# Kernel tuning notes

Hardware: AMD Instinct MI355X
Metric: run time of the kernel (lower is better)

Reference implementation:

```python
import math
import jax, jax.numpy as jnp
import numpy as np

B, T, C, H, V = 2, 512, 768, 12, 50304
HD = C // H
EPS_LN = 1e-5
SINK_ITERS = 6           # MAX_ITER_SINK
N_STEPS = 20             # ceil((1-0)/h_max), h_max=0.05
H_STEP = 1.0 / N_STEPS   # Euler step size h


def layer_norm(x, w, b):
    mu = jnp.mean(x, axis=-1, keepdims=True)
    var = jnp.mean(jnp.square(x - mu), axis=-1, keepdims=True)
    return (x - mu) * jax.lax.rsqrt(var + EPS_LN) * w + b


def sinkhorn_pi(Cmat):
    # log-domain Sinkhorn (eps=1) on cost matrix Cmat [N, T, T]; returns transport plan pi
    n = Cmat.shape[-1]
    log_marg = -jnp.log(jnp.asarray(n, Cmat.dtype))  # log(1/n), uniform marginals
    u = jnp.zeros(Cmat.shape[:-1], Cmat.dtype)
    v = jnp.zeros(Cmat.shape[:-1], Cmat.dtype)
    def M(u, v):
        return -Cmat + u[..., :, None] + v[..., None, :]
    for _ in range(SINK_ITERS):
        u = (log_marg - jax.nn.logsumexp(M(u, v), axis=-1)) + u
        v = (log_marg - jax.nn.logsumexp(M(u, v), axis=-2)) + v
    return jnp.exp(M(u, v))


def block_f(z, t, attn_ln_w, attn_ln_b, c_attn_w, c_attn_b, c_proj_w, c_proj_b,
            mlp_ln_w, mlp_ln_b, c_fc_w, c_fc_b, mlp_proj_w, mlp_proj_b):
    Bz, Tz, Cz = z.shape
    tcol = jnp.full((Bz, Tz, 1), t, z.dtype)
    # attention sub-block: LN over C+1 dims (x concat time)
    x = layer_norm(jnp.concatenate([z, tcol], axis=-1), attn_ln_w, attn_ln_b)
    qkv = x @ c_attn_w + c_attn_b                      # [B,T,3C]
    q, k, v = jnp.split(qkv, 3, axis=-1)
    q = q.reshape(Bz, Tz, H, HD).transpose(0, 2, 1, 3)  # [B,H,T,hd]
    k = k.reshape(Bz, Tz, H, HD).transpose(0, 2, 1, 3)
    v = v.reshape(Bz, Tz, H, HD).transpose(0, 2, 1, 3)
    att = jnp.einsum('bhqd,bhkd->bhqk', q, k) * (1.0 / math.sqrt(HD))
    mask = jnp.tril(jnp.ones((Tz, Tz), dtype=bool))
    att = jax.nn.softmax(jnp.where(mask, att, -jnp.inf), axis=-1)
    pi = sinkhorn_pi(att.reshape(Bz * H, Tz, Tz)) * Tz  # sink(att)[0] * n
    y = jnp.einsum('bhqk,bhkd->bhqd', pi.reshape(Bz, H, Tz, Tz), v)
    y = y.transpose(0, 2, 1, 3).reshape(Bz, Tz, Cz)
    y = y @ c_proj_w + c_proj_b
    # MLP sub-block on LN(concat(attn_out, t))
    ht = layer_norm(jnp.concatenate([y, tcol], axis=-1), mlp_ln_w, mlp_ln_b)
    h1 = jax.nn.gelu(ht @ c_fc_w + c_fc_b, approximate=False)
    return h1 @ mlp_proj_w + mlp_proj_b


def setup_inputs() -> dict:
    key = jax.random.key(0)
    ks = jax.random.split(key, 8)
    s = 0.02
    return {
        'idx': jax.random.randint(ks[0], (B, T), 0, V),
        'wte': s * jax.random.normal(ks[1], (V, C), jnp.float32),
        'wpe': s * jax.random.normal(ks[2], (T, C), jnp.float32),
        'attn_ln_w': jnp.ones((C + 1,), jnp.float32),
        'attn_ln_b': jnp.zeros((C + 1,), jnp.float32),
        'c_attn_w': s * jax.random.normal(ks[3], (C + 1, 3 * C), jnp.float32),
        'c_attn_b': jnp.zeros((3 * C,), jnp.float32),
        'c_proj_w': s * jax.random.normal(ks[4], (C, C), jnp.float32),
        'c_proj_b': jnp.zeros((C,), jnp.float32),
        'mlp_ln_w': jnp.ones((C + 1,), jnp.float32),
        'mlp_ln_b': jnp.zeros((C + 1,), jnp.float32),
        'c_fc_w': s * jax.random.normal(ks[5], (C + 1, 4 * C), jnp.float32),
        'c_fc_b': jnp.zeros((4 * C,), jnp.float32),
        'mlp_proj_w': s * jax.random.normal(ks[6], (4 * C, C), jnp.float32),
        'mlp_proj_b': jnp.zeros((C,), jnp.float32),
        'lnf_w': jnp.ones((C,), jnp.float32),
        'lnf_b': jnp.zeros((C,), jnp.float32),
    }


def reference(idx, wte, wpe, attn_ln_w, attn_ln_b, c_attn_w, c_attn_b, c_proj_w,
              c_proj_b, mlp_ln_w, mlp_ln_b, c_fc_w, c_fc_b, mlp_proj_w, mlp_proj_b,
              lnf_w, lnf_b):
    x = wte[idx] + wpe[jnp.arange(idx.shape[1])]  # [B,T,C]

    def step(carry, _):
        z, t = carry
        dz = block_f(z, t, attn_ln_w, attn_ln_b, c_attn_w, c_attn_b, c_proj_w,
                     c_proj_b, mlp_ln_w, mlp_ln_b, c_fc_w, c_fc_b, mlp_proj_w,
                     mlp_proj_b)
        return (z + H_STEP * dz, t + H_STEP), None

    (x, _), _ = jax.lax.scan(step, (x, jnp.float32(0.0)), None, length=N_STEPS)
    x = layer_norm(x, lnf_w, lnf_b)
    logits = x[:, -1:, :] @ wte.T  # inference path: last position only, tied head
    return logits
```

## Files before the change

kernel.cpp:

```cpp
#include <hip/hip_runtime.h>
#include <hip/hip_bf16.h>
#include <math.h>

typedef unsigned short ushortT;
typedef unsigned int uintT;

#define Bc   2
#define Tc   512
#define Cc   768
#define Hc   12
#define HDc  64
#define Vc   50304
#define BTc  (Bc*Tc)
#define NHc  (Bc*Hc)
#define C3   (3*Cc)
#define C4   (4*Cc)
#define EPS_LN 1e-5f
#define H_STEP 0.05f
#define INVN (1.0f/512.0f)
#define SB   4
#define ELP  (Tc + 8)
#define VLP  136

typedef float f32x4 __attribute__((ext_vector_type(4)));
typedef __bf16 bf16x8 __attribute__((ext_vector_type(8)));
typedef ushortT us8 __attribute__((ext_vector_type(8)));
typedef uintT u32x4 __attribute__((ext_vector_type(4)));

__device__ __forceinline__ ushortT f2bf(float f) {
    union { float f; unsigned u; } x; x.f = f;
    unsigned r = (x.u + 0x7fffu + ((x.u >> 16) & 1u)) >> 16;
    return (ushortT)r;
}
__device__ __forceinline__ float bf2f(ushortT b) {
    union { unsigned u; float f; } x; x.u = ((unsigned)b) << 16;
    return x.f;
}
__device__ __forceinline__ float bflo(uintT w) {
    union { unsigned u; float f; } x; x.u = w << 16;
    return x.f;
}
__device__ __forceinline__ float bfhi(uintT w) {
    union { unsigned u; float f; } x; x.u = w & 0xffff0000u;
    return x.f;
}

__device__ __forceinline__ void gll16(const ushortT* g, ushortT* l) {
    __builtin_amdgcn_global_load_lds(
        (const __attribute__((address_space(1))) unsigned int*)g,
        (__attribute__((address_space(3))) unsigned int*)l,
        16, 0, 0);
}

__device__ __forceinline__ float waveReduceSumX(float v) {
    for (int o = 32; o; o >>= 1) v += __shfl_xor(v, o);
    return v;
}
__device__ __forceinline__ float blockReduceSum(float v) {
    __shared__ float sm[4];
    for (int o = 32; o; o >>= 1) v += __shfl_down(v, o);
    __syncthreads();
    if ((threadIdx.x & 63) == 0) sm[threadIdx.x >> 6] = v;
    __syncthreads();
    return sm[0] + sm[1] + sm[2] + sm[3];
}

__global__ __launch_bounds__(256)
void wtrans_kernel(const float* __restrict__ W, ushortT* __restrict__ out,
                   int K, int N)
{
    __shared__ float t[32][33];
    int k0 = blockIdx.x * 32, n0 = blockIdx.y * 32;
    int tx = threadIdx.x & 31, ty = threadIdx.x >> 5;
    for (int r = ty; r < 32; r += 8)
        t[r][tx] = W[(size_t)(k0 + r) * N + n0 + tx];
    __syncthreads();
    for (int r = ty; r < 32; r += 8)
        out[(size_t)(n0 + r) * K + k0 + tx] = f2bf(t[tx][r]);
}

__global__ __launch_bounds__(256)
void embed_ln(const int* __restrict__ idx, const float* __restrict__ wte,
              const float* __restrict__ wpe, float* __restrict__ z,
              const float* __restrict__ lnw, const float* __restrict__ lnb,
              ushortT* __restrict__ xlnb, float* __restrict__ xt)
{
    int row = blockIdx.x, tid = threadIdx.x;
    int tok = idx[row];
    float v[3];
#pragma unroll
    for (int q = 0; q < 3; ++q) {
        int c = tid + 256 * q;
        float val = wte[(size_t)tok * Cc + c] + wpe[(size_t)(row & (Tc - 1)) * Cc + c];
        z[(size_t)row * Cc + c] = val;
        v[q] = val;
    }
    float s = blockReduceSum(v[0] + v[1] + v[2]);
    float mu = s / 769.f;
    float d0 = v[0] - mu, d1 = v[1] - mu, d2 = v[2] - mu;
    float ss = blockReduceSum(d0 * d0 + d1 * d1 + d2 * d2);
    float dt = 0.f - mu;
    float var = (ss + dt * dt) / 769.f;
    float rs = rsqrtf(var + EPS_LN);
#pragma unroll
    for (int q = 0; q < 3; ++q) {
        int c = tid + 256 * q;
        xlnb[(size_t)row * Cc + c] = f2bf((v[q] - mu) * rs * lnw[c] + lnb[c]);
    }
    if (tid == 0) xt[row] = dt * rs * lnw[Cc] + lnb[Cc];
}

__global__ __launch_bounds__(256)
void ln_kernel(const void* __restrict__ X, const float* __restrict__ w,
               const float* __restrict__ bb, void* __restrict__ Y,
               float* __restrict__ yt, int hasT, float tval,
               int rowMul, int rowAdd, int obf16, int ibf16)
{
    int orow = blockIdx.x;
    int r = orow * rowMul + rowAdd;
    int tid = threadIdx.x;
    float xv[3];
    if (ibf16) {
        const ushortT* x = (const ushortT*)X + (size_t)r * Cc;
#pragma unroll
        for (int q = 0; q < 3; ++q) xv[q] = bf2f(x[tid + 256 * q]);
    } else {
        const float* x = (const float*)X + (size_t)r * Cc;
#pragma unroll
        for (int q = 0; q < 3; ++q) xv[q] = x[tid + 256 * q];
    }
    float s = blockReduceSum(xv[0] + xv[1] + xv[2]);
    float cnt = hasT ? 769.f : 768.f;
    float mu = (s + (hasT ? tval : 0.f)) / cnt;
    float d0 = xv[0] - mu, d1 = xv[1] - mu, d2 = xv[2] - mu;
    float ss = blockReduceSum(d0 * d0 + d1 * d1 + d2 * d2);
    float dt = tval - mu;
    float var = (ss + (hasT ? dt * dt : 0.f)) / cnt;
    float rs = rsqrtf(var + EPS_LN);
#pragma unroll
    for (int q = 0; q < 3; ++q) {
        int c = tid + 256 * q;
        float v = (xv[q] - mu) * rs * w[c] + bb[c];
        if (obf16) ((ushortT*)Y)[(size_t)orow * Cc + c] = f2bf(v);
        else       ((float*)Y)[(size_t)orow * Cc + c] = v;
    }
    if (hasT && tid == 0) yt[orow] = dt * rs * w[Cc] + bb[Cc];
}

template <int EPI>
__global__ __launch_bounds__(256)
void gemm_bt(const ushortT* __restrict__ A, int lda,
             const ushortT* __restrict__ Bt, int ldb,
             void* __restrict__ Cm, int ldc, int K,
             const float* __restrict__ bias,
             const float* __restrict__ extraA,
             const float* __restrict__ extraB)
{
    __shared__ __align__(16) ushortT Als[128 * 64];
    __shared__ __align__(16) ushortT Bls[128 * 64];
    if (EPI == 4) {
        int koff = blockIdx.z * K;
        A += koff; Bt += koff;
    }
    int tid = threadIdx.x;
    int lane = tid & 63, wid = tid >> 6;
    int wm = wid >> 1, wn = wid & 1;
    int m0 = blockIdx.y * 128, n0 = blockIdx.x * 128;
    f32x4 acc[4][4];
    const f32x4 fz = {0.f, 0.f, 0.f, 0.f};
#pragma unroll
    for (int i = 0; i < 4; ++i)
#pragma unroll
        for (int j = 0; j < 4; ++j) acc[i][j] = fz;

    for (int k0 = 0; k0 < K; k0 += 64) {
#pragma unroll
        for (int is = 0; is < 4; ++is) {
            int ch = is * 256 + tid;
            int m = ch >> 3;
            int kc8 = (ch & 7) ^ (m & 7);
            gll16(A + (size_t)(m0 + m) * lda + k0 + kc8 * 8, Als + ch * 8);
            gll16(Bt + (size_t)(n0 + m) * ldb + k0 + kc8 * 8, Bls + ch * 8);
        }
        __syncthreads();
#pragma unroll
        for (int kk = 0; kk < 2; ++kk) {
            int cidx = kk * 4 + (lane >> 4);
            bf16x8 af[4], bfv[4];
#pragma unroll
            for (int i = 0; i < 4; ++i) {
                int row = wm * 64 + i * 16 + (lane & 15);
                af[i] = *(const bf16x8*)(Als + ((size_t)row * 8 + (cidx ^ (row & 7))) * 8);
                int col = wn * 64 + i * 16 + (lane & 15);
                bfv[i] = *(const bf16x8*)(Bls + ((size_t)col * 8 + (cidx ^ (col & 7))) * 8);
            }
#pragma unroll
            for (int i = 0; i < 4; ++i)
#pragma unroll
                for (int j = 0; j < 4; ++j)
                    acc[i][j] = __builtin_amdgcn_mfma_f32_16x16x32_bf16(af[i], bfv[j], acc[i][j], 0, 0, 0);
        }
        __syncthreads();
    }
#pragma unroll
    for (int i = 0; i < 4; ++i) {
#pragma unroll
        for (int j = 0; j < 4; ++j) {
#pragma unroll
            for (int r = 0; r < 4; ++r) {
                int row = m0 + wm * 64 + i * 16 + (lane >> 4) * 4 + r;
                int col = n0 + wn * 64 + j * 16 + (lane & 15);
                float v = acc[i][j][r];
                if (extraA) v += extraA[row] * extraB[col];
                if (bias) v += bias[col];
                size_t oi = (size_t)row * ldc + col;
                if (EPI == 0) {
                    ((ushortT*)Cm)[oi] = f2bf(v);
                } else if (EPI == 1) {
                    v = 0.5f * v * (1.f + erff(v * 0.70710678118654752440f));
                    ((ushortT*)Cm)[oi] = f2bf(v);
                } else if (EPI == 4) {
                    ((float*)Cm)[(size_t)blockIdx.z * ((size_t)BTc * Cc) + oi] = v;
                }
            }
        }
    }
}

__global__ __launch_bounds__(512)
void sinkfused(const ushortT* __restrict__ qkvb, ushortT* __restrict__ y,
               float* __restrict__ partials, unsigned* __restrict__ ctr,
               unsigned barBase)
{
    int gb = blockIdx.x;
    int n = gb % NHc, r = gb / NHc;
    int row0 = r * 128;
    int b = n / Hc, h = n - b * Hc;
    int tid = threadIdx.x;
    int l = tid & 63, w = tid >> 6;
    __shared__ __align__(16) ushortT Els[128][ELP];
    __shared__ __align__(16) ushortT Kshare[64 * VLP];
    __shared__ float a_s[128];
    __shared__ float b_s[Tc];
    const f32x4 fz = {0.f, 0.f, 0.f, 0.f};

    int qrow = b * Tc + row0 + w * 16 + (l & 15);
    const ushortT* qp = qkvb + (size_t)qrow * C3 + h * HDc + (l >> 4) * 8;
    bf16x8 aq0 = *(const bf16x8*)(qp);
    bf16x8 aq1 = *(const bf16x8*)(qp + 32);

    int kcmax = r + 1;
    f32x4 acc[32];
#pragma unroll
    for (int j = 0; j < 32; ++j) acc[j] = fz;

    ushortT* EK = &Els[0][0];
    {
        int nch = kcmax * 1024;
        for (int ch = tid; ch < nch; ch += 512) {
            int row = ch >> 3, c16 = (ch & 7) ^ (row & 7);
            gll16(qkvb + (size_t)(b * Tc + row) * C3 + Cc + h * HDc + c16 * 8,
                  EK + ch * 8);
        }
    }
    __syncthreads();
#pragma unroll
    for (int kc = 0; kc < 4; ++kc) {
        if (kc < kcmax) {
#pragma unroll
            for (int jj = 0; jj < 8; ++jj) {
                int krow = kc * 128 + jj * 16 + (l & 15);
                int c16a = (l >> 4);
                int c16b = 4 + (l >> 4);
                bf16x8 bk0 = *(const bf16x8*)(EK + ((size_t)krow * 8 + (c16a ^ (krow & 7))) * 8);
                bf16x8 bk1 = *(const bf16x8*)(EK + ((size_t)krow * 8 + (c16b ^ (krow & 7))) * 8);
                acc[kc * 8 + jj] = __builtin_amdgcn_mfma_f32_16x16x32_bf16(aq0, bk0, acc[kc * 8 + jj], 0, 0, 0);
                acc[kc * 8 + jj] = __builtin_amdgcn_mfma_f32_16x16x32_bf16(aq1, bk1, acc[kc * 8 + jj], 0, 0, 0);
            }
        }
    }
    __syncthreads();

    int nvalid = kcmax * 8;
    int colbase = (l & 15);
    int rowa[4];
#pragma unroll
    for (int e = 0; e < 4; ++e) rowa[e] = row0 + w * 16 + (l >> 4) * 4 + e;

    float mx[4] = {-INFINITY, -INFINITY, -INFINITY, -INFINITY};
#pragma unroll
    for (int j = 0; j < 32; ++j) {
        if (j < nvalid) {
            int col = j * 16 + colbase;
#pragma unroll
            for (int e = 0; e < 4; ++e)
                if (col <= rowa[e]) mx[e] = fmaxf(mx[e], acc[j][e] * 0.125f);
        }
    }
#pragma unroll
    for (int e = 0; e < 4; ++e)
        for (int o = 1; o < 16; o <<= 1) mx[e] = fmaxf(mx[e], __shfl_xor(mx[e], o));

    float se[4] = {0.f, 0.f, 0.f, 0.f};
#pragma unroll
    for (int j = 0; j < 32; ++j) {
        if (j < nvalid) {
            int col = j * 16 + colbase;
#pragma unroll
            for (int e = 0; e < 4; ++e) {
                float exv = (col <= rowa[e]) ? __expf(acc[j][e] * 0.125f - mx[e]) : 0.f;
                acc[j][e] = exv;
                se[e] += exv;
            }
        }
    }
#pragma unroll
    for (int e = 0; e < 4; ++e)
        for (int o = 1; o < 16; o <<= 1) se[e] += __shfl_xor(se[e], o);
    float inv[4];
#pragma unroll
    for (int e = 0; e < 4; ++e) inv[e] = 1.f / se[e];

    float rsum[4] = {0.f, 0.f, 0.f, 0.f};
#pragma unroll
    for (int j = 0; j < 32; ++j) {
        if (j < nvalid) {
            int col = j * 16 + colbase;
#pragma unroll
            for (int e = 0; e < 4; ++e) {
                float Ee = __expf(-(acc[j][e] * inv[e]));
                rsum[e] += Ee;
                Els[w * 16 + (l >> 4) * 4 + e][col] = f2bf(Ee);
            }
        }
    }
#pragma unroll
    for (int e = 0; e < 4; ++e) {
        for (int o = 1; o < 16; o <<= 1) rsum[e] += __shfl_xor(rsum[e], o);
        if ((l & 15) == 0)
            a_s[w * 16 + (l >> 4) * 4 + e] = INVN / (rsum[e] + (float)(Tc - nvalid * 16));
    }
    {
        int tailc = 64 - kcmax * 16;
        if (tailc > 0) {
            us8 ones8;
#pragma unroll
            for (int e = 0; e < 8; ++e) ones8[e] = 0x3F80;
            for (int idx2 = l; idx2 < 16 * tailc; idx2 += 64) {
                int rr = idx2 / tailc, cc = idx2 - rr * tailc;
                *(us8*)&Els[w * 16 + rr][(kcmax * 16 + cc) * 8] = ones8;
            }
        }
    }
    __syncthreads();

    float* mypart = partials + (size_t)(n * SB + r) * Tc;
    const float* hpart = partials + (size_t)n * SB * Tc;
    unsigned* myctr = ctr + n * 16;
    float* scr = (float*)Kshare;

#pragma unroll 1
    for (int p = 0; p < 11; ++p) {
        if ((p & 1) == 0) {
            int cg = tid & 63, sl = tid >> 6;
            float ac[8] = {0.f, 0.f, 0.f, 0.f, 0.f, 0.f, 0.f, 0.f};
#pragma unroll
            for (int i = 0; i < 16; ++i) {
                int row = sl * 16 + i;
                us8 ev = *(const us8*)&Els[row][cg * 8];
                float fa = a_s[row];
#pragma unroll
                for (int e = 0; e < 8; ++e)
                    ac[e] += bf2f(ev[e]) * fa;
            }
            f32x4 lo = {ac[0], ac[1], ac[2], ac[3]};
            f32x4 hi = {ac[4], ac[5], ac[6], ac[7]};
            *(f32x4*)&scr[sl * 512 + cg * 8] = lo;
            *(f32x4*)&scr[sl * 512 + cg * 8 + 4] = hi;
            __syncthreads();
            int j = tid;
            float accs = 0.f;
#pragma unroll
            for (int s2 = 0; s2 < 8; ++s2) accs += scr[s2 * 512 + j];
            __hip_atomic_store(&mypart[j], accs, __ATOMIC_RELAXED, __HIP_MEMORY_SCOPE_AGENT);
            __syncthreads();
            if (tid == 0) {
                __threadfence();
                atomicAdd(myctr, 1u);
                unsigned tgt = barBase + (unsigned)(p / 2 + 1) * SB;
                while (__hip_atomic_load(myctr, __ATOMIC_ACQUIRE, __HIP_MEMORY_SCOPE_AGENT) < tgt)
                    __builtin_amdgcn_s_sleep(2);
            }
            __syncthreads();
            float s0 = __hip_atomic_load(&hpart[j], __ATOMIC_RELAXED, __HIP_MEMORY_SCOPE_AGENT);
            float s1 = __hip_atomic_load(&hpart[Tc + j], __ATOMIC_RELAXED, __HIP_MEMORY_SCOPE_AGENT);
            float s2 = __hip_atomic_load(&hpart[2 * Tc + j], __ATOMIC_RELAXED, __HIP_MEMORY_SCOPE_AGENT);
            float s3 = __hip_atomic_load(&hpart[3 * Tc + j], __ATOMIC_RELAXED, __HIP_MEMORY_SCOPE_AGENT);
            b_s[j] = INVN / (s0 + s1 + s2 + s3);
            __syncthreads();
        } else {
            f32x4 b0 = *(const f32x4*)&b_s[l * 8];
            f32x4 b1 = *(const f32x4*)&b_s[l * 8 + 4];
            float breg[8] = {b0[0], b0[1], b0[2], b0[3], b1[0], b1[1], b1[2], b1[3]};
#pragma unroll 1
            for (int k = 0; k < 16; k += 4) {
                int r0 = w * 16 + k;
                u32x4 q0 = *(const u32x4*)(&Els[r0 + 0][l * 8]);
                u32x4 q1 = *(const u32x4*)(&Els[r0 + 1][l * 8]);
                u32x4 q2 = *(const u32x4*)(&Els[r0 + 2][l * 8]);
                u32x4 q3 = *(const u32x4*)(&Els[r0 + 3][l * 8]);
                float s0 = 0.f, s1 = 0.f, s2 = 0.f, s3 = 0.f;
#pragma unroll
                for (int c = 0; c < 4; ++c) {
                    s0 += bflo(q0[c]) * breg[2 * c] + bfhi(q0[c]) * breg[2 * c + 1];
                    s1 += bflo(q1[c]) * breg[2 * c] + bfhi(q1[c]) * breg[2 * c + 1];
                    s2 += bflo(q2[c]) * breg[2 * c] + bfhi(q2[c]) * breg[2 * c + 1];
                    s3 += bflo(q3[c]) * breg[2 * c] + bfhi(q3[c]) * breg[2 * c + 1];
                }
                s0 = waveReduceSumX(s0);
                s1 = waveReduceSumX(s1);
                s2 = waveReduceSumX(s2);
                s3 = waveReduceSumX(s3);
                if (l == 0) {
                    a_s[r0 + 0] = INVN / s0;
                    a_s[r0 + 1] = INVN / s1;
                    a_s[r0 + 2] = INVN / s2;
                    a_s[r0 + 3] = INVN / s3;
                }
            }
            __syncthreads();
        }
    }

    {
        ushortT* Kls2 = Kshare;
        int wm = w >> 1, wn = w & 1;
        f32x4 acc2[2][2];
#pragma unroll
        for (int i = 0; i < 2; ++i)
#pragma unroll
            for (int j = 0; j < 2; ++j) acc2[i][j] = fz;
        const ushortT* vbase = qkvb + (size_t)(b * Tc) * C3 + 2 * Cc + h * HDc;

#pragma unroll 1
        for (int k0 = 0; k0 < Tc; k0 += 128) {
#pragma unroll
            for (int ii = 0; ii < 2; ++ii) {
                int ch = ii * 512 + tid;
                int tt = ch >> 3, dblk = ch & 7;
                us8 vv = *(const us8*)(vbase + (size_t)(k0 + tt) * C3 + dblk * 8);
                float bs = 512.f * b_s[k0 + tt];
#pragma unroll
                for (int e = 0; e < 8; ++e)
                    Kls2[(dblk * 8 + e) * VLP + tt] = f2bf(bf2f(vv[e]) * bs);
            }
            __syncthreads();
#pragma unroll
            for (int kk = 0; kk < 128; kk += 32) {
                bf16x8 af[2], bv[2];
#pragma unroll
                for (int i = 0; i < 2; ++i)
                    af[i] = *(const bf16x8*)&Els[wm * 32 + i * 16 + (l & 15)][k0 + kk + (l >> 4) * 8];
#pragma unroll
                for (int j = 0; j < 2; ++j)
                    bv[j] = *(const bf16x8*)(Kls2 + (size_t)(wn * 32 + j * 16 + (l & 15)) * VLP + kk + (l >> 4) * 8);
#pragma unroll
                for (int i = 0; i < 2; ++i)
#pragma unroll
                    for (int j = 0; j < 2; ++j)
                        acc2[i][j] = __builtin_amdgcn_mfma_f32_16x16x32_bf16(af[i], bv[j], acc2[i][j], 0, 0, 0);
            }
            __syncthreads();
        }
#pragma unroll
        for (int i = 0; i < 2; ++i)
#pragma unroll
            for (int j = 0; j < 2; ++j)
#pragma unroll
                for (int rr = 0; rr < 4; ++rr) {
                    int lrow = wm * 32 + i * 16 + (l >> 4) * 4 + rr;
                    float a_r = a_s[lrow];
                    int grow = b * Tc + row0 + lrow;
                    int gcol = h * HDc + wn * 32 + j * 16 + (l & 15);
                    y[(size_t)grow * Cc + gcol] = f2bf(acc2[i][j][rr] * a_r);
                }
    }
}

__global__ __launch_bounds__(256)
void reduce_ln(const float* __restrict__ parts, const float* __restrict__ bias,
               float* __restrict__ z, const float* __restrict__ lnw,
               const float* __restrict__ lnb, ushortT* __restrict__ xlnb,
               float* __restrict__ xt, float tval, int doEuler)
{
    int row = blockIdx.x, tid = threadIdx.x;
    const size_t CS = (size_t)BTc * Cc;
    float v[3];
#pragma unroll
    for (int q = 0; q < 3; ++q) {
        int c = tid + 256 * q;
        size_t idx = (size_t)row * Cc + c;
        float s = parts[idx] + parts[CS + idx] + parts[2 * CS + idx]
                + parts[3 * CS + idx] + bias[c];
        if (doEuler) {
            v[q] = z[idx] + H_STEP * s;
            z[idx] = v[q];
        } else {
            v[q] = s;
        }
    }
    float s = blockReduceSum(v[0] + v[1] + v[2]);
    float mu = (s + tval) / 769.f;
    float d0 = v[0] - mu, d1 = v[1] - mu, d2 = v[2] - mu;
    float ss = blockReduceSum(d0 * d0 + d1 * d1 + d2 * d2);
    float dt = tval - mu;
    float var = (ss + dt * dt) / 769.f;
    float rs = rsqrtf(var + EPS_LN);
#pragma unroll
    for (int q = 0; q < 3; ++q) {
        int c = tid + 256 * q;
        xlnb[(size_t)row * Cc + c] = f2bf((v[q] - mu) * rs * lnw[c] + lnb[c]);
    }
    if (tid == 0) xt[row] = dt * rs * lnw[Cc] + lnb[Cc];
}

__global__ __launch_bounds__(256)
void logits_kernel(const float* __restrict__ xf, const float* __restrict__ wte,
                   float* __restrict__ out)
{
    __shared__ __align__(16) float xs[2 * Cc];
    int tid = threadIdx.x;
    for (int i = tid; i < 384; i += 256)
        ((f32x4*)xs)[i] = ((const f32x4*)xf)[i];
    __syncthreads();
    int w = tid >> 6, lane = tid & 63;
    int vrow = blockIdx.x * 4 + w;
    const f32x4* wr = (const f32x4*)(wte + (size_t)vrow * Cc);
    const f32x4* x0 = (const f32x4*)xs;
    const f32x4* x1 = (const f32x4*)(xs + Cc);
    float a0 = 0.f, a1 = 0.f;
#pragma unroll
    for (int it = 0; it < 3; ++it) {
        int k4 = it * 64 + lane;
        f32x4 wv = wr[k4];
        f32x4 p = x0[k4], q = x1[k4];
        a0 += wv[0] * p[0] + wv[1] * p[1] + wv[2] * p[2] + wv[3] * p[3];
        a1 += wv[0] * q[0] + wv[1] * q[1] + wv[2] * q[2] + wv[3] * q[3];
    }
    for (int o = 32; o; o >>= 1) {
        a0 += __shfl_down(a0, o);
        a1 += __shfl_down(a1, o);
    }
    if (lane == 0) {
        out[vrow] = a0;
        out[Vc + vrow] = a1;
    }
}

extern "C" void kernel_launch(void* const* d_in, const int* in_sizes, int n_in,
                              void* d_out, int out_size, void* d_ws, size_t ws_size,
                              hipStream_t stream)
{
    const int*   idx        = (const int*)  d_in[0];
    const float* wte        = (const float*)d_in[1];
    const float* wpe        = (const float*)d_in[2];
    const float* attn_ln_w  = (const float*)d_in[3];
    const float* attn_ln_b  = (const float*)d_in[4];
    const float* c_attn_w   = (const float*)d_in[5];
    const float* c_attn_b   = (const float*)d_in[6];
    const float* c_proj_w   = (const float*)d_in[7];
    const float* c_proj_b   = (const float*)d_in[8];
    const float* mlp_ln_w   = (const float*)d_in[9];
    const float* mlp_ln_b   = (const float*)d_in[10];
    const float* c_fc_w     = (const float*)d_in[11];
    const float* c_fc_b     = (const float*)d_in[12];
    const float* mlp_proj_w = (const float*)d_in[13];
    const float* mlp_proj_b = (const float*)d_in[14];
    const float* lnf_w      = (const float*)d_in[15];
    const float* lnf_b      = (const float*)d_in[16];
    float* out = (float*)d_out;

    char* base = (char*)d_ws;
    size_t off = 0;
    auto alloc = [&](size_t bytes) -> void* {
        void* p = base + off;
        off = (off + bytes + 255) & ~(size_t)255;
        return p;
    };
    float*   z     = (float*)  alloc((size_t)BTc * Cc * 4);
    float*   parts = (float*)  alloc((size_t)4 * BTc * Cc * 4);
    ushortT* qkvb  = (ushortT*)alloc((size_t)BTc * C3 * 2);
    ushortT* xlnb  = (ushortT*)alloc((size_t)BTc * Cc * 2);
    ushortT* y     = (ushortT*)alloc((size_t)BTc * Cc * 2);
    ushortT* h1    = (ushortT*)alloc((size_t)BTc * C4 * 2);
    float*   xt    = (float*)  alloc(BTc * 4);
    float*   partv = (float*)  alloc((size_t)NHc * SB * Tc * 4);
    unsigned* ctr  = (unsigned*)alloc(NHc * 16 * 4);
    float*   xf    = (float*)  alloc(2 * Cc * 4);
    ushortT* WqkvT = (ushortT*)alloc((size_t)C3 * Cc * 2);
    ushortT* WprojT= (ushortT*)alloc((size_t)Cc * Cc * 2);
    ushortT* WfcT  = (ushortT*)alloc((size_t)C4 * Cc * 2);
    ushortT* WmlpT = (ushortT*)alloc((size_t)Cc * C4 * 2);

    hipMemsetAsync(ctr, 0, NHc * 16 * 4, stream);
    embed_ln<<<BTc, 256, 0, stream>>>(idx, wte, wpe, z, attn_ln_w, attn_ln_b, xlnb, xt);
    wtrans_kernel<<<dim3(Cc / 32, C3 / 32), 256, 0, stream>>>(c_attn_w,   WqkvT,  Cc, C3);
    wtrans_kernel<<<dim3(Cc / 32, Cc / 32), 256, 0, stream>>>(c_proj_w,   WprojT, Cc, Cc);
    wtrans_kernel<<<dim3(Cc / 32, C4 / 32), 256, 0, stream>>>(c_fc_w,     WfcT,   Cc, C4);
    wtrans_kernel<<<dim3(C4 / 32, Cc / 32), 256, 0, stream>>>(mlp_proj_w, WmlpT,  C4, Cc);

    float t = 0.f;
    for (int step = 0; step < 20; ++step) {
        gemm_bt<0><<<dim3(C3 / 128, BTc / 128), 256, 0, stream>>>(
            xlnb, Cc, WqkvT, Cc, qkvb, C3, Cc,
            c_attn_b, xt, c_attn_w + (size_t)Cc * C3);
        sinkfused<<<NHc * SB, 512, 0, stream>>>(
            qkvb, y, partv, ctr, (unsigned)(step * 6 * SB));
        gemm_bt<4><<<dim3(Cc / 128, BTc / 128, 4), 256, 0, stream>>>(
            y, Cc, WprojT, Cc, parts, Cc, Cc / 4,
            nullptr, nullptr, nullptr);
        reduce_ln<<<BTc, 256, 0, stream>>>(parts, c_proj_b, nullptr,
                                           mlp_ln_w, mlp_ln_b, xlnb, xt, t, 0);
        gemm_bt<1><<<dim3(C4 / 128, BTc / 128), 256, 0, stream>>>(
            xlnb, Cc, WfcT, Cc, h1, C4, Cc,
            c_fc_b, xt, c_fc_w + (size_t)Cc * C4);
        gemm_bt<4><<<dim3(Cc / 128, BTc / 128, 4), 256, 0, stream>>>(
            h1, C4, WmlpT, C4, parts, Cc, C4 / 4,
            nullptr, nullptr, nullptr);
        t += H_STEP;
        reduce_ln<<<BTc, 256, 0, stream>>>(parts, mlp_proj_b, z,
                                           attn_ln_w, attn_ln_b, xlnb, xt, t, 1);
    }

    ln_kernel<<<2, 256, 0, stream>>>(z, lnf_w, lnf_b, xf, nullptr, 0, 0.f, Tc, Tc - 1, 0, 0);
    logits_kernel<<<Vc / 4, 256, 0, stream>>>(xf, wte, out);
}
```

Baseline: 3.426 ms.

## Split Sinkhorn kernel into 64-row strips across 8 blocks per head

```diff
diff --git a/kernel.cpp b/kernel.cpp
--- a/kernel.cpp
+++ b/kernel.cpp
@@ -18,7 +18,7 @@
 #define EPS_LN 1e-5f
 #define H_STEP 0.05f
 #define INVN (1.0f/512.0f)
-#define SB   4
+#define SBQ  8
 #define ELP  (Tc + 8)
 #define VLP  136
 
@@ -234,29 +234,31 @@
 {
     int gb = blockIdx.x;
     int n = gb % NHc, r = gb / NHc;
-    int row0 = r * 128;
+    int row0 = r * 64;
     int b = n / Hc, h = n - b * Hc;
     int tid = threadIdx.x;
     int l = tid & 63, w = tid >> 6;
-    __shared__ __align__(16) ushortT Els[128][ELP];
+    int wm = w >> 1, wn = w & 1;
+    __shared__ __align__(16) ushortT Els[64][ELP];
     __shared__ __align__(16) ushortT Kshare[64 * VLP];
-    __shared__ float a_s[128];
+    __shared__ float a_s[64];
     __shared__ float b_s[Tc];
+    __shared__ float smx[2][64], ssum[2][64], srs[2][64];
     const f32x4 fz = {0.f, 0.f, 0.f, 0.f};
 
-    int qrow = b * Tc + row0 + w * 16 + (l & 15);
+    int qrow = b * Tc + row0 + wm * 16 + (l & 15);
     const ushortT* qp = qkvb + (size_t)qrow * C3 + h * HDc + (l >> 4) * 8;
     bf16x8 aq0 = *(const bf16x8*)(qp);
     bf16x8 aq1 = *(const bf16x8*)(qp + 32);
 
-    int kcmax = r + 1;
-    f32x4 acc[32];
-#pragma unroll
-    for (int j = 0; j < 32; ++j) acc[j] = fz;
+    int nT2 = (r + 1) * 2;
+    f32x4 acc[16];
+#pragma unroll
+    for (int j = 0; j < 16; ++j) acc[j] = fz;
 
     ushortT* EK = &Els[0][0];
     {
-        int nch = kcmax * 1024;
+        int nch = (r + 1) * 512;
         for (int ch = tid; ch < nch; ch += 512) {
             int row = ch >> 3, c16 = (ch & 7) ^ (row & 7);
             gll16(qkvb + (size_t)(b * Tc + row) * C3 + Cc + h * HDc + c16 * 8,
@@ -265,51 +267,55 @@
     }
     __syncthreads();
 #pragma unroll
-    for (int kc = 0; kc < 4; ++kc) {
-        if (kc < kcmax) {
-#pragma unroll
-            for (int jj = 0; jj < 8; ++jj) {
-                int krow = kc * 128 + jj * 16 + (l & 15);
-                int c16a = (l >> 4);
-                int c16b = 4 + (l >> 4);
-                bf16x8 bk0 = *(const bf16x8*)(EK + ((size_t)krow * 8 + (c16a ^ (krow & 7))) * 8);
-                bf16x8 bk1 = *(const bf16x8*)(EK + ((size_t)krow * 8 + (c16b ^ (krow & 7))) * 8);
-                acc[kc * 8 + jj] = __builtin_amdgcn_mfma_f32_16x16x32_bf16(aq0, bk0, acc[kc * 8 + jj], 0, 0, 0);
-                acc[kc * 8 + jj] = __builtin_amdgcn_mfma_f32_16x16x32_bf16(aq1, bk1, acc[kc * 8 + jj], 0, 0, 0);
-            }
-        }
-    }
-    __syncthreads();
-
-    int nvalid = kcmax * 8;
+    for (int t = 0; t < 16; ++t) {
+        if (t < nT2) {
+            int krow = (2 * t + wn) * 16 + (l & 15);
+            int c16a = (l >> 4);
+            int c16b = 4 + (l >> 4);
+            bf16x8 bk0 = *(const bf16x8*)(EK + ((size_t)krow * 8 + (c16a ^ (krow & 7))) * 8);
+            bf16x8 bk1 = *(const bf16x8*)(EK + ((size_t)krow * 8 + (c16b ^ (krow & 7))) * 8);
+            acc[t] = __builtin_amdgcn_mfma_f32_16x16x32_bf16(aq0, bk0, acc[t], 0, 0, 0);
+            acc[t] = __builtin_amdgcn_mfma_f32_16x16x32_bf16(aq1, bk1, acc[t], 0, 0, 0);
+        }
+    }
+    __syncthreads();
+
     int colbase = (l & 15);
+    int lrow4 = wm * 16 + (l >> 4) * 4;
     int rowa[4];
 #pragma unroll
-    for (int e = 0; e < 4; ++e) rowa[e] = row0 + w * 16 + (l >> 4) * 4 + e;
+    for (int e = 0; e < 4; ++e) rowa[e] = row0 + lrow4 + e;
 
     float mx[4] = {-INFINITY, -INFINITY, -INFINITY, -INFINITY};
 #pragma unroll
-    for (int j = 0; j < 32; ++j) {
-        if (j < nvalid) {
-            int col = j * 16 + colbase;
+    for (int t = 0; t < 16; ++t) {
+        if (t < nT2) {
+            int col = (2 * t + wn) * 16 + colbase;
 #pragma unroll
             for (int e = 0; e < 4; ++e)
-                if (col <= rowa[e]) mx[e] = fmaxf(mx[e], acc[j][e] * 0.125f);
+                if (col <= rowa[e]) mx[e] = fmaxf(mx[e], acc[t][e] * 0.125f);
         }
     }
 #pragma unroll
     for (int e = 0; e < 4; ++e)
         for (int o = 1; o < 16; o <<= 1) mx[e] = fmaxf(mx[e], __shfl_xor(mx[e], o));
+    if ((l & 15) == 0)
+#pragma unroll
+        for (int e = 0; e < 4; ++e) smx[wn][lrow4 + e] = mx[e];
+    __syncthreads();
+#pragma unroll
+    for (int e = 0; e < 4; ++e)
+        mx[e] = fmaxf(smx[0][lrow4 + e], smx[1][lrow4 + e]);
 
     float se[4] = {0.f, 0.f, 0.f, 0.f};
 #pragma unroll
-    for (int j = 0; j < 32; ++j) {
-        if (j < nvalid) {
-            int col = j * 16 + colbase;
+    for (int t = 0; t < 16; ++t) {
+        if (t < nT2) {
+            int col = (2 * t + wn) * 16 + colbase;
 #pragma unroll
             for (int e = 0; e < 4; ++e) {
-                float exv = (col <= rowa[e]) ? __expf(acc[j][e] * 0.125f - mx[e]) : 0.f;
-                acc[j][e] = exv;
+                float exv = (col <= rowa[e]) ? __expf(acc[t][e] * 0.125f - mx[e]) : 0.f;
+                acc[t][e] = exv;
                 se[e] += exv;
             }
         }
@@ -317,45 +323,57 @@
 #pragma unroll
     for (int e = 0; e < 4; ++e)
         for (int o = 1; o < 16; o <<= 1) se[e] += __shfl_xor(se[e], o);
+    if ((l & 15) == 0)
+#pragma unroll
+        for (int e = 0; e < 4; ++e) ssum[wn][lrow4 + e] = se[e];
+    __syncthreads();
     float inv[4];
 #pragma unroll
-    for (int e = 0; e < 4; ++e) inv[e] = 1.f / se[e];
+    for (int e = 0; e < 4; ++e)
+        inv[e] = 1.f / (ssum[0][lrow4 + e] + ssum[1][lrow4 + e]);
 
     float rsum[4] = {0.f, 0.f, 0.f, 0.f};
 #pragma unroll
-    for (int j = 0; j < 32; ++j) {
-        if (j < nvalid) {
-            int col = j * 16 + colbase;
+    for (int t = 0; t < 16; ++t) {
+        if (t < nT2) {
+            int col = (2 * t + wn) * 16 + colbase;
 #pragma unroll
             for (int e = 0; e < 4; ++e) {
-                float Ee = __expf(-(acc[j][e] * inv[e]));
+                float Ee = __expf(-(acc[t][e] * inv[e]));
                 rsum[e] += Ee;
-                Els[w * 16 + (l >> 4) * 4 + e][col] = f2bf(Ee);
-            }
-        }
-    }
-#pragma unroll
-    for (int e = 0; e < 4; ++e) {
+                Els[lrow4 + e][col] = f2bf(Ee);
+            }
+        }
+    }
+#pragma unroll
+    for (int e = 0; e < 4; ++e)
         for (int o = 1; o < 16; o <<= 1) rsum[e] += __shfl_xor(rsum[e], o);
-        if ((l & 15) == 0)
-            a_s[w * 16 + (l >> 4) * 4 + e] = INVN / (rsum[e] + (float)(Tc - nvalid * 16));
+    if ((l & 15) == 0)
+#pragma unroll
+        for (int e = 0; e < 4; ++e) srs[wn][lrow4 + e] = rsum[e];
+    __syncthreads();
+    if (wn == 0 && (l & 15) == 0) {
+        float tail = (float)(Tc - (r + 1) * 64);
+#pragma unroll
+        for (int e = 0; e < 4; ++e)
+            a_s[lrow4 + e] = INVN / (srs[0][lrow4 + e] + srs[1][lrow4 + e] + tail);
     }
     {
-        int tailc = 64 - kcmax * 16;
+        int tailc = 64 - (r + 1) * 8;
         if (tailc > 0) {
             us8 ones8;
 #pragma unroll
             for (int e = 0; e < 8; ++e) ones8[e] = 0x3F80;
-            for (int idx2 = l; idx2 < 16 * tailc; idx2 += 64) {
+            for (int idx2 = tid; idx2 < 64 * tailc; idx2 += 512) {
                 int rr = idx2 / tailc, cc = idx2 - rr * tailc;
-                *(us8*)&Els[w * 16 + rr][(kcmax * 16 + cc) * 8] = ones8;
-            }
-        }
-    }
-    __syncthreads();
-
-    float* mypart = partials + (size_t)(n * SB + r) * Tc;
-    const float* hpart = partials + (size_t)n * SB * Tc;
+                *(us8*)&Els[rr][((r + 1) * 8 + cc) * 8] = ones8;
+            }
+        }
+    }
+    __syncthreads();
+
+    float* mypart = partials + (size_t)(n * SBQ + r) * Tc;
+    const float* hpart = partials + (size_t)n * SBQ * Tc;
     unsigned* myctr = ctr + n * 16;
     float* scr = (float*)Kshare;
 
@@ -365,8 +383,8 @@
             int cg = tid & 63, sl = tid >> 6;
             float ac[8] = {0.f, 0.f, 0.f, 0.f, 0.f, 0.f, 0.f, 0.f};
 #pragma unroll
-            for (int i = 0; i < 16; ++i) {
-                int row = sl * 16 + i;
+            for (int i = 0; i < 8; ++i) {
+                int row = sl * 8 + i;
                 us8 ev = *(const us8*)&Els[row][cg * 8];
                 float fa = a_s[row];
 #pragma unroll
@@ -387,24 +405,24 @@
             if (tid == 0) {
                 __threadfence();
                 atomicAdd(myctr, 1u);
-                unsigned tgt = barBase + (unsigned)(p / 2 + 1) * SB;
+                unsigned tgt = barBase + (unsigned)(p / 2 + 1) * SBQ;
                 while (__hip_atomic_load(myctr, __ATOMIC_ACQUIRE, __HIP_MEMORY_SCOPE_AGENT) < tgt)
                     __builtin_amdgcn_s_sleep(2);
             }
             __syncthreads();
-            float s0 = __hip_atomic_load(&hpart[j], __ATOMIC_RELAXED, __HIP_MEMORY_SCOPE_AGENT);
-            float s1 = __hip_atomic_load(&hpart[Tc + j], __ATOMIC_RELAXED, __HIP_MEMORY_SCOPE_AGENT);
-            float s2 = __hip_atomic_load(&hpart[2 * Tc + j], __ATOMIC_RELAXED, __HIP_MEMORY_SCOPE_AGENT);
-            float s3 = __hip_atomic_load(&hpart[3 * Tc + j], __ATOMIC_RELAXED, __HIP_MEMORY_SCOPE_AGENT);
-            b_s[j] = INVN / (s0 + s1 + s2 + s3);
+            float accs2 = 0.f;
+#pragma unroll
+            for (int s2 = 0; s2 < SBQ; ++s2)
+                accs2 += __hip_atomic_load(&hpart[s2 * Tc + j], __ATOMIC_RELAXED, __HIP_MEMORY_SCOPE_AGENT);
+            b_s[j] = INVN / accs2;
             __syncthreads();
         } else {
             f32x4 b0 = *(const f32x4*)&b_s[l * 8];
             f32x4 b1 = *(const f32x4*)&b_s[l * 8 + 4];
             float breg[8] = {b0[0], b0[1], b0[2], b0[3], b1[0], b1[1], b1[2], b1[3]};
 #pragma unroll 1
-            for (int k = 0; k < 16; k += 4) {
-                int r0 = w * 16 + k;
+            for (int k = 0; k < 8; k += 4) {
+                int r0 = w * 8 + k;
                 u32x4 q0 = *(const u32x4*)(&Els[r0 + 0][l * 8]);
                 u32x4 q1 = *(const u32x4*)(&Els[r0 + 1][l * 8]);
                 u32x4 q2 = *(const u32x4*)(&Els[r0 + 2][l * 8]);
@@ -434,12 +452,9 @@
 
     {
         ushortT* Kls2 = Kshare;
-        int wm = w >> 1, wn = w & 1;
-        f32x4 acc2[2][2];
-#pragma unroll
-        for (int i = 0; i < 2; ++i)
-#pragma unroll
-            for (int j = 0; j < 2; ++j) acc2[i][j] = fz;
+        f32x4 acc2[2];
+#pragma unroll
+        for (int j = 0; j < 2; ++j) acc2[j] = fz;
         const ushortT* vbase = qkvb + (size_t)(b * Tc) * C3 + 2 * Cc + h * HDc;
 
 #pragma unroll 1
@@ -457,33 +472,25 @@
             __syncthreads();
 #pragma unroll
             for (int kk = 0; kk < 128; kk += 32) {
-                bf16x8 af[2], bv[2];
-#pragma unroll
-                for (int i = 0; i < 2; ++i)
-                    af[i] = *(const bf16x8*)&Els[wm * 32 + i * 16 + (l & 15)][k0 + kk + (l >> 4) * 8];
-#pragma unroll
-                for (int j = 0; j < 2; ++j)
-                    bv[j] = *(const bf16x8*)(Kls2 + (size_t)(wn * 32 + j * 16 + (l & 15)) * VLP + kk + (l >> 4) * 8);
-#pragma unroll
-                for (int i = 0; i < 2; ++i)
-#pragma unroll
-                    for (int j = 0; j < 2; ++j)
-                        acc2[i][j] = __builtin_amdgcn_mfma_f32_16x16x32_bf16(af[i], bv[j], acc2[i][j], 0, 0, 0);
+                bf16x8 af = *(const bf16x8*)&Els[wm * 16 + (l & 15)][k0 + kk + (l >> 4) * 8];
+#pragma unroll
+                for (int j = 0; j < 2; ++j) {
+                    bf16x8 bv = *(const bf16x8*)(Kls2 + (size_t)(wn * 32 + j * 16 + (l & 15)) * VLP + kk + (l >> 4) * 8);
+                    acc2[j] = __builtin_amdgcn_mfma_f32_16x16x32_bf16(af, bv, acc2[j], 0, 0, 0);
+                }
             }
             __syncthreads();
         }
 #pragma unroll
-        for (int i = 0; i < 2; ++i)
-#pragma unroll
-            for (int j = 0; j < 2; ++j)
-#pragma unroll
-                for (int rr = 0; rr < 4; ++rr) {
-                    int lrow = wm * 32 + i * 16 + (l >> 4) * 4 + rr;
-                    float a_r = a_s[lrow];
-                    int grow = b * Tc + row0 + lrow;
-                    int gcol = h * HDc + wn * 32 + j * 16 + (l & 15);
-                    y[(size_t)grow * Cc + gcol] = f2bf(acc2[i][j][rr] * a_r);
-                }
+        for (int j = 0; j < 2; ++j)
+#pragma unroll
+            for (int rr = 0; rr < 4; ++rr) {
+                int lrow = wm * 16 + (l >> 4) * 4 + rr;
+                float a_r = a_s[lrow];
+                int grow = b * Tc + row0 + lrow;
+                int gcol = h * HDc + wn * 32 + j * 16 + (l & 15);
+                y[(size_t)grow * Cc + gcol] = f2bf(acc2[j][rr] * a_r);
+            }
     }
 }
 
@@ -594,7 +601,7 @@
     ushortT* y     = (ushortT*)alloc((size_t)BTc * Cc * 2);
     ushortT* h1    = (ushortT*)alloc((size_t)BTc * C4 * 2);
     float*   xt    = (float*)  alloc(BTc * 4);
-    float*   partv = (float*)  alloc((size_t)NHc * SB * Tc * 4);
+    float*   partv = (float*)  alloc((size_t)NHc * SBQ * Tc * 4);
     unsigned* ctr  = (unsigned*)alloc(NHc * 16 * 4);
     float*   xf    = (float*)  alloc(2 * Cc * 4);
     ushortT* WqkvT = (ushortT*)alloc((size_t)C3 * Cc * 2);
@@ -614,8 +621,8 @@
         gemm_bt<0><<<dim3(C3 / 128, BTc / 128), 256, 0, stream>>>(
             xlnb, Cc, WqkvT, Cc, qkvb, C3, Cc,
             c_attn_b, xt, c_attn_w + (size_t)Cc * C3);
-        sinkfused<<<NHc * SB, 512, 0, stream>>>(
-            qkvb, y, partv, ctr, (unsigned)(step * 6 * SB));
+        sinkfused<<<NHc * SBQ, 512, 0, stream>>>(
+            qkvb, y, partv, ctr, (unsigned)(step * 6 * SBQ));
         gemm_bt<4><<<dim3(Cc / 128, BTc / 128, 4), 256, 0, stream>>>(
             y, Cc, WprojT, Cc, parts, Cc, Cc / 4,
             nullptr, nullptr, nullptr);
```

New measurement: 3.404 ms (median of 2 runs). No clear change (-0.7%).
